# Kernel optimization log

Hardware: AMD Instinct MI355X
Metric: run time of the kernel (lower is better)

The kernel has to match this reference:

```python
import math
import jax, jax.numpy as jnp
import numpy as np

HOP = 256
N_FFT = 1024
SR = 24000
B = 8
T = 1200          # feature frames
L = T * HOP       # 307200 audio samples
K_REV = 8192
BINS = N_FFT // 2 + 1


def setup_inputs() -> dict:
    key = jax.random.key(0)
    k1, k2, k3, k4, k5 = jax.random.split(key, 5)
    # realistic voiced f0 in [50, 400] Hz (forward gates on f0 > 20 Hz)
    f0 = 50.0 + 350.0 * jax.random.uniform(k1, (B, T), dtype=jnp.float32)
    env_per = jax.random.uniform(k2, (B, BINS, T), dtype=jnp.float32)
    env_noi = 0.1 * jax.random.uniform(k3, (B, BINS, T), dtype=jnp.float32)
    rev = 0.01 * jax.random.normal(k4, (B, K_REV), dtype=jnp.float32)
    # stands in for torch.rand_like(imp) inside forward (uniform [0,1))
    noi = jax.random.uniform(k5, (B, L), dtype=jnp.float32)
    # periodic Hann window, as torch.hann_window(n_fft)
    window = (0.5 - 0.5 * jnp.cos(2.0 * jnp.pi * jnp.arange(N_FFT) / N_FFT)).astype(jnp.float32)
    return {"f0": f0, "env_per": env_per, "env_noi": env_noi, "rev": rev, "noi": noi, "window": window}


def _interp_linear(x, scale):
    # torch F.interpolate(mode='linear', align_corners=False)
    Lx = x.shape[-1]
    out_len = Lx * scale
    src = (jnp.arange(out_len, dtype=jnp.float32) + 0.5) / scale - 0.5
    src = jnp.clip(src, 0.0, Lx - 1)
    i0 = jnp.floor(src).astype(jnp.int32)
    i1 = jnp.minimum(i0 + 1, Lx - 1)
    w = src - i0.astype(jnp.float32)
    return x[:, i0] * (1.0 - w) + x[:, i1] * w


def _stft(x, window):
    # torch.stft(center=True, pad_mode='reflect', return_complex=True)
    pad = N_FFT // 2
    xp = jnp.pad(x, ((0, 0), (pad, pad)), mode='reflect')
    n_frames = 1 + (xp.shape[-1] - N_FFT) // HOP
    idx = jnp.arange(n_frames)[:, None] * HOP + jnp.arange(N_FFT)[None, :]
    frames = xp[:, idx] * window                      # [B, F, N_FFT]
    return jnp.fft.rfft(frames, axis=-1).transpose(0, 2, 1)  # [B, BINS, F]


def _istft(spec, window):
    # torch.istft(center=True): windowed overlap-add with window-square normalization
    frames = jnp.fft.irfft(spec.transpose(0, 2, 1), n=N_FFT, axis=-1) * window  # [B, F, N_FFT]
    Bc, Fr, _ = frames.shape
    out_len = N_FFT + HOP * (Fr - 1)
    idx = (jnp.arange(Fr)[:, None] * HOP + jnp.arange(N_FFT)[None, :]).reshape(-1)
    out = jnp.zeros((Bc, out_len), frames.dtype).at[:, idx].add(frames.reshape(Bc, -1))
    wsq = jnp.zeros((out_len,), frames.dtype).at[idx].add(jnp.tile(window ** 2, Fr))
    out = out / jnp.where(wsq > 1e-11, wsq, 1.0)
    pad = N_FFT // 2
    return out[:, pad:out_len - pad]


def _min_phase(amp, eps=1e-5):
    # homomorphic minimum-phase reconstruction from real amplitude envelope
    # amp: [B, BINS, F]  ->  complex spectrum exp(rfft(lifted real cepstrum))
    log_amp = jnp.log(jnp.maximum(amp, eps))
    cep = jnp.fft.irfft(log_amp, n=N_FFT, axis=1)     # [B, N_FFT, F] real cepstrum
    lift = jnp.concatenate([
        jnp.ones((1,), jnp.float32),
        2.0 * jnp.ones((N_FFT // 2 - 1,), jnp.float32),
        jnp.ones((1,), jnp.float32),
        jnp.zeros((N_FFT // 2 - 1,), jnp.float32),
    ])
    return jnp.exp(jnp.fft.rfft(cep * lift[None, :, None], axis=1))  # [B, BINS, F]


def _fft_convolve(signal, kernel):
    # DDSP-style FFT convolution: zero-pad signal right, kernel left, multiply spectra
    Ls = signal.shape[-1]
    sig = jnp.pad(signal, ((0, 0), (0, Ls)))
    ker = jnp.pad(kernel, ((0, 0), (2 * Ls - kernel.shape[-1], 0)))
    out = jnp.fft.irfft(jnp.fft.rfft(sig) * jnp.fft.rfft(ker), n=2 * Ls)
    return out[:, Ls:]


def reference(f0, env_per, env_noi, rev, noi, window):
    env_per = jnp.pad(env_per, ((0, 0), (0, 0), (1, 0)))   # [B, BINS, T+1]
    env_noi = jnp.pad(env_noi, ((0, 0), (0, 0), (1, 0)))
    # sample-rate f0 track and impulse amplitude scale
    f0_up = _interp_linear(f0, HOP)                        # [B, L]
    imp_scale = jax.lax.rsqrt(jnp.maximum(f0_up, 20.0)) * math.sqrt(SR)
    # impulse train: fire where the running phase wraps past an integer
    phase = jnp.cumsum(f0_up, axis=-1) / SR
    saw = jnp.mod(phase, 1.0)
    imp = (saw - jnp.roll(saw, 1, axis=-1) < 0.0).astype(jnp.float32)
    imp = imp.at[:, 0].set(0.0)
    imp = imp * imp_scale
    imp_stft = _stft(imp, window)                          # [B, BINS, T+1]
    noi_stft = _stft(noi, window)
    # voiced/unvoiced gating of the periodic envelope
    mask = (jnp.pad(f0, ((0, 0), (1, 0)))[:, None, :] > 20.0).astype(jnp.float32)
    env_per = env_per * mask
    voi_stft = imp_stft * _min_phase(env_per) + noi_stft * env_noi
    voi = _istft(voi_stft, window)                         # [B, L]
    voi = _fft_convolve(voi, rev)                          # [B, L]
    return voi
```

## Files before the change

### kernel.cpp

```cpp
#include <hip/hip_runtime.h>
#include <math.h>

#define BB 8
#define TT 1200
#define NFFT 1024
#define BINS 513
#define LTOT 307200
#define KREV 8192
#define NFRM 34
#define NSAMP 8960
#define OUTOFF 299008
#define SQRT_SR 154.91933384829668f

#define OFF_FR   0

__device__ __forceinline__ int rev10(int n) { return (int)(__brev((unsigned)n) >> 22); }

__device__ __forceinline__ void dit1024(float* re, float* im,
                                        const float* twr, const float* twi,
                                        float dir, int tid) {
#pragma unroll
    for (int s = 1; s <= 10; ++s) {
        const int half = 1 << (s - 1);
        __syncthreads();
        int q = tid;
        int t = q & (half - 1);
        int i0 = ((q >> (s - 1)) << s) | t;
        int i1 = i0 + half;
        float wr = twr[half - 1 + t];
        float wi = dir * twi[half - 1 + t];
        float br = re[i1], bi = im[i1];
        float vr = fmaf(br, wr, -(bi * wi));
        float vi = fmaf(br, wi, bi * wr);
        float ar = re[i0], ai = im[i0];
        re[i0] = ar + vr; im[i0] = ai + vi;
        re[i1] = ar - vr; im[i1] = ai - vi;
    }
    __syncthreads();
}

__device__ __forceinline__ void dif1024(float* re, float* im,
                                        const float* twr, const float* twi,
                                        float dir, int tid) {
#pragma unroll
    for (int s = 10; s >= 1; --s) {
        const int half = 1 << (s - 1);
        __syncthreads();
        int q = tid;
        int t = q & (half - 1);
        int i0 = ((q >> (s - 1)) << s) | t;
        int i1 = i0 + half;
        float wr = twr[half - 1 + t];
        float wi = dir * twi[half - 1 + t];
        float ar = re[i0], ai = im[i0];
        float br = re[i1], bi = im[i1];
        re[i0] = ar + br; im[i0] = ai + bi;
        float dr = ar - br, di = ai - bi;
        re[i1] = fmaf(dr, wr, -(di * wi));
        im[i1] = fmaf(dr, wi, di * wr);
    }
    __syncthreads();
}

#define LV1 0
#define LV2 4480
#define LV3 6720
#define LV4 7840
#define LV5 8400
#define LV6 8680
#define LV7 8820
#define LV8 8890
#define LV9 8925
#define LV10 8942
#define LV11 8950
#define LV12 8954
#define LV13 8956

__global__ __launch_bounds__(512) void kfrm(const float* __restrict__ f0,
                                            const float* __restrict__ env_per,
                                            const float* __restrict__ env_noi,
                                            const float* __restrict__ noi,
                                            const float* __restrict__ win,
                                            float* __restrict__ W,
                                            float* __restrict__ out) {
    const int bid = blockIdx.x;
    const int tid = threadIdx.x;
    const int b = bid / 17;
    const int fp = (bid - b * 17) * 2;
    const int fg = fp + 1;

    __shared__ __align__(16) float SMEM[17917];
    __shared__ float cw[1281], fw[1281];
    __shared__ float twr[1023], twi[1023];

    {
        float4* out4 = (float4*)out;
        int g = bid * 512 + tid;
        for (int idx = g; idx < (BB * LTOT) / 4; idx += 136 * 512)
            out4[idx] = make_float4(0.f, 0.f, 0.f, 0.f);
    }
    for (int x = tid; x < 1023; x += 512) {
        int hb = 31 - __clz(x + 1);
        int half = 1 << hb;
        int t = (x + 1) - half;
        float a = 3.14159265358979323846f * ((float)t / (float)half);
        float sv, cv; sincosf(a, &sv, &cv);
        twr[x] = cv; twi[x] = sv;
    }

    float* F = SMEM;
    float* L = SMEM + 8960;
    for (int i = tid; i < NSAMP; i += 512) {
        float src = __fsub_rn(__fdiv_rn(__fadd_rn((float)i, 0.5f), 256.0f), 0.5f);
        src = fminf(fmaxf(src, 0.0f), (float)(TT - 1));
        int i0 = (int)floorf(src);
        int i1 = i0 + 1; if (i1 > TT - 1) i1 = TT - 1;
        float w = __fsub_rn(src, (float)i0);
        float a0 = __fmul_rn(f0[b * TT + i0], __fsub_rn(1.0f, w));
        float a1 = __fmul_rn(f0[b * TT + i1], w);
        F[i] = __fadd_rn(a0, a1);
    }
    __syncthreads();
    for (int j = tid; j < 4480; j += 512) L[LV1 + j] = __fadd_rn(F[2*j], F[2*j+1]);
    __syncthreads();
    for (int j = tid; j < 2240; j += 512) L[LV2 + j] = __fadd_rn(L[LV1 + 2*j], L[LV1 + 2*j+1]);
    __syncthreads();
    for (int j = tid; j < 1120; j += 512) L[LV3 + j] = __fadd_rn(L[LV2 + 2*j], L[LV2 + 2*j+1]);
    __syncthreads();
    for (int j = tid; j < 560; j += 512)  L[LV4 + j] = __fadd_rn(L[LV3 + 2*j], L[LV3 + 2*j+1]);
    __syncthreads();
    for (int j = tid; j < 280; j += 512)  L[LV5 + j] = __fadd_rn(L[LV4 + 2*j], L[LV4 + 2*j+1]);
    __syncthreads();
    if (tid < 140) L[LV6 + tid] = __fadd_rn(L[LV5 + 2*tid], L[LV5 + 2*tid+1]);
    __syncthreads();
    if (tid < 70)  L[LV7 + tid] = __fadd_rn(L[LV6 + 2*tid], L[LV6 + 2*tid+1]);
    __syncthreads();
    if (tid < 35)  L[LV8 + tid] = __fadd_rn(L[LV7 + 2*tid], L[LV7 + 2*tid+1]);
    __syncthreads();
    if (tid < 17)  L[LV9 + tid] = __fadd_rn(L[LV8 + 2*tid], L[LV8 + 2*tid+1]);
    __syncthreads();
    if (tid < 8)   L[LV10 + tid] = __fadd_rn(L[LV9 + 2*tid], L[LV9 + 2*tid+1]);
    __syncthreads();
    if (tid < 4)   L[LV11 + tid] = __fadd_rn(L[LV10 + 2*tid], L[LV10 + 2*tid+1]);
    __syncthreads();
    if (tid < 2)   L[LV12 + tid] = __fadd_rn(L[LV11 + 2*tid], L[LV11 + 2*tid+1]);
    __syncthreads();
    if (tid < 1)   L[LV13 + tid] = __fadd_rn(L[LV12 + 0], L[LV12 + 1]);
    __syncthreads();
    const int cbase = (fp >= 3) ? (256 * fp - 513) : 0;
    {
        const int offs[14] = {0, LV1, LV2, LV3, LV4, LV5, LV6, LV7, LV8, LV9, LV10, LV11, LV12, LV13};
        for (int w = tid; w < 1281; w += 512) {
            int p = cbase + w;
            if (p < NSAMP) {
                int n = p + 1;
                float acc = 0.f; int pos = 0; bool first = true;
#pragma unroll
                for (int k = 13; k >= 1; --k) {
                    if ((n >> k) & 1) {
                        float t = L[offs[k] + (pos >> k)];
                        acc = first ? t : __fadd_rn(acc, t);
                        first = false;
                        pos += (1 << k);
                    }
                }
                if (n & 1) {
                    float t = F[pos];
                    acc = first ? t : __fadd_rn(acc, t);
                }
                cw[w] = acc;
                fw[w] = F[p];
            }
        }
    }
    __syncthreads();

    float* wr_  = SMEM;
    float* wi_  = SMEM + 1024;
    float* zfr  = SMEM + 2048;
    float* zfi  = SMEM + 3072;
    float* zgr  = SMEM + 4096;
    float* zgi  = SMEM + 5120;
    float* mpfr = SMEM + 6144;
    float* mpfi = SMEM + 6660;
    float* mpgr = SMEM + 7176;
    float* mpgi = SMEM + 7692;

    for (int k = tid; k < BINS; k += 512) {
        float epf = 0.0f;
        if (fp > 0) {
            float f0v = f0[b * TT + (fp - 1)];
            epf = (f0v > 20.0f) ? env_per[(size_t)(b * BINS + k) * TT + (fp - 1)] : 0.0f;
        }
        float f0g = f0[b * TT + (fg - 1)];
        float epg = (f0g > 20.0f) ? env_per[(size_t)(b * BINS + k) * TT + (fg - 1)] : 0.0f;
        mpfr[k] = logf(fmaxf(epf, 1e-5f));
        mpgr[k] = logf(fmaxf(epg, 1e-5f));
    }
    __syncthreads();
#pragma unroll
    for (int r = 0; r < 2; ++r) {
        int n = tid + 512 * r;
        int kv = (n <= 512) ? n : 1024 - n;
        float a = mpfr[kv], bb2 = mpgr[kv];
        __syncthreads();
        wr_[n] = a;
        wi_[n] = bb2;
    }
    dif1024(wr_, wi_, twr, twi, -1.f, tid);
    const float inv = 1.0f / 1024.0f;
#pragma unroll
    for (int r = 0; r < 2; ++r) {
        int p = tid + 512 * r;
        int n = rev10(p);
        float wgt = (n == 0 || n == 512) ? inv : ((n < 512) ? 2.0f * inv : 0.0f);
        wr_[p] *= wgt;
        wi_[p] *= wgt;
    }
    dit1024(wr_, wi_, twr, twi, -1.f, tid);
    for (int k = tid; k < BINS; k += 512) {
        int mk = (1024 - k) & 1023;
        float yr = wr_[k], yi = wi_[k];
        float ymr = wr_[mk], ymi = -wi_[mk];
        float Lfr = 0.5f * (yr + ymr), Lfi = 0.5f * (yi + ymi);
        float dr = yr - ymr, di = yi - ymi;
        float Lgr = 0.5f * di, Lgi = -0.5f * dr;
        float ef = expf(Lfr);
        mpfr[k] = ef * cosf(Lfi); mpfi[k] = ef * sinf(Lfi);
        float eg = expf(Lgr);
        mpgr[k] = eg * cosf(Lgi); mpgi[k] = eg * sinf(Lgi);
    }
    __syncthreads();
#pragma unroll
    for (int r = 0; r < 2; ++r) {
        int n = tid + 512 * r;
        int i = 256 * fp + n - 512; if (i < 0) i = -i;
        float v = 0.0f;
        if (i > 0) {
            int iw = i - cbase;
            float ph  = __fdiv_rn(cw[iw], 24000.0f);
            float sw  = __fsub_rn(ph, floorf(ph));
            float ph2 = __fdiv_rn(cw[iw - 1], 24000.0f);
            float sw2 = __fsub_rn(ph2, floorf(ph2));
            if (__fsub_rn(sw, sw2) < 0.0f)
                v = __fmul_rn(__fdiv_rn(1.0f, __fsqrt_rn(fmaxf(fw[iw], 20.0f))), SQRT_SR);
        }
        float wv = win[n];
        zfr[n] = __fmul_rn(noi[b * LTOT + i], wv);
        zfi[n] = __fmul_rn(v, wv);
        int i2 = 256 * fg + n - 512; if (i2 < 0) i2 = -i2;
        float v2 = 0.0f;
        if (i2 > 0) {
            int iw = i2 - cbase;
            float ph  = __fdiv_rn(cw[iw], 24000.0f);
            float sw  = __fsub_rn(ph, floorf(ph));
            float ph2 = __fdiv_rn(cw[iw - 1], 24000.0f);
            float sw2 = __fsub_rn(ph2, floorf(ph2));
            if (__fsub_rn(sw, sw2) < 0.0f)
                v2 = __fmul_rn(__fdiv_rn(1.0f, __fsqrt_rn(fmaxf(fw[iw], 20.0f))), SQRT_SR);
        }
        zgr[n] = __fmul_rn(noi[b * LTOT + i2], wv);
        zgi[n] = __fmul_rn(v2, wv);
    }
    dif1024(zfr, zfi, twr, twi, -1.f, tid);
    dif1024(zgr, zgi, twr, twi, -1.f, tid);
#pragma unroll
    for (int r = 0; r < 2; ++r) {
        int p = tid + 512 * r;
        int k = rev10(p);
        int kk = (k <= 512) ? k : 1024 - k;
        bool cj = (k > 512);
        int p1 = rev10(kk);
        int p2 = rev10((1024 - kk) & 1023);
        float vr, vi;
        {
            float z1r = zfr[p1], z1i = zfi[p1];
            float z2r = zfr[p2], z2i = -zfi[p2];
            float Nr = 0.5f * (z1r + z2r), Ni = 0.5f * (z1i + z2i);
            float dr = z1r - z2r, di = z1i - z2i;
            float Ir = 0.5f * di, Ii = -0.5f * dr;
            float mpr = mpfr[kk], mpi2 = mpfi[kk];
            float en = (fp == 0) ? 0.f : env_noi[(size_t)(b * BINS + kk) * TT + (fp - 1)];
            vr = Ir * mpr - Ii * mpi2 + Nr * en;
            vi = Ir * mpi2 + Ii * mpr + Ni * en;
            if (cj) vi = -vi;
        }
        float vgr, vgi;
        {
            float z1r = zgr[p1], z1i = zgi[p1];
            float z2r = zgr[p2], z2i = -zgi[p2];
            float Nr = 0.5f * (z1r + z2r), Ni = 0.5f * (z1i + z2i);
            float dr = z1r - z2r, di = z1i - z2i;
            float Ir = 0.5f * di, Ii = -0.5f * dr;
            float mpr = mpgr[kk], mpi2 = mpgi[kk];
            float en = env_noi[(size_t)(b * BINS + kk) * TT + (fg - 1)];
            vgr = Ir * mpr - Ii * mpi2 + Nr * en;
            vgi = Ir * mpi2 + Ii * mpr + Ni * en;
            if (cj) vgi = -vgi;
        }
        __syncthreads();
        wr_[p] = vr - vgi;
        wi_[p] = vi + vgr;
    }
    dit1024(wr_, wi_, twr, twi, +1.f, tid);
#pragma unroll
    for (int r = 0; r < 2; ++r) {
        int n = tid + 512 * r;
        float wv = win[n];
        W[OFF_FR + (((size_t)(b * NFRM + fp)) << 10) + n] = __fmul_rn(__fmul_rn(wr_[n], inv), wv);
        W[OFF_FR + (((size_t)(b * NFRM + fg)) << 10) + n] = __fmul_rn(__fmul_rn(wi_[n], inv), wv);
    }
}

__global__ __launch_bounds__(256) void k4(const float* __restrict__ rev,
                                          const float* __restrict__ win,
                                          const float* __restrict__ W,
                                          float* __restrict__ out) {
    const int tid = threadIdx.x;
    const int b = blockIdx.x / 72;
    int r = blockIdx.x - b * 72;
    int jt = 0, acc0 = 0;
    while (acc0 + 2 * (jt + 1) <= r) { acc0 += 2 * (jt + 1); ++jt; }
    const int mc = r - acc0;
    const int j0 = jt << 10, m0 = mc << 9;

    __shared__ __align__(16) float S[1536];
    const int base = j0 - m0 - 512;
    for (int x = tid; x < 1536; x += 256) {
        int j = base + x;
        float v = 0.f;
        if (j >= 0 && j < KREV) {
            int s = j + 512;
            int flo = (s >= 1023) ? ((s - 1023 + 255) >> 8) : 0;
            int fhi = s >> 8; if (fhi > NFRM - 1) fhi = NFRM - 1;
            float acc = 0.f, wsq = 0.f;
            for (int f = flo; f <= fhi; ++f) {
                int o = s - (f << 8);
                acc = __fadd_rn(acc, W[OFF_FR + (((size_t)(b * NFRM + f)) << 10) + o]);
                float wv = win[o];
                wsq = __fadd_rn(wsq, __fmul_rn(wv, wv));
            }
            float den = (wsq > 1e-11f) ? wsq : 1.0f;
            v = __fdiv_rn(acc, den);
        }
        S[x] = v;
    }
    __syncthreads();

    const float4* S4 = (const float4*)S;
    const float* Rb = rev + b * KREV + m0;
    float y0 = 0.f, y1 = 0.f, y2 = 0.f, y3 = 0.f;
    const int qi = tid + 128;
    float4 Bv = S4[qi];
#pragma unroll 4
    for (int mq = 0; mq < 128; ++mq) {
        float4 A = S4[qi - 1 - mq];
        float4 r4 = *(const float4*)(Rb + 4 * mq);
        y0 = fmaf(r4.x, Bv.x, y0); y0 = fmaf(r4.y, A.w,  y0); y0 = fmaf(r4.z, A.z,  y0); y0 = fmaf(r4.w, A.y,  y0);
        y1 = fmaf(r4.x, Bv.y, y1); y1 = fmaf(r4.y, Bv.x, y1); y1 = fmaf(r4.z, A.w,  y1); y1 = fmaf(r4.w, A.z,  y1);
        y2 = fmaf(r4.x, Bv.z, y2); y2 = fmaf(r4.y, Bv.y, y2); y2 = fmaf(r4.z, Bv.x, y2); y2 = fmaf(r4.w, A.w,  y2);
        y3 = fmaf(r4.x, Bv.w, y3); y3 = fmaf(r4.y, Bv.z, y3); y3 = fmaf(r4.z, Bv.y, y3); y3 = fmaf(r4.w, Bv.x, y3);
        Bv = A;
    }
    float* o = out + (size_t)b * LTOT + OUTOFF + j0 + 4 * tid;
    atomicAdd(o + 0, y0);
    atomicAdd(o + 1, y1);
    atomicAdd(o + 2, y2);
    atomicAdd(o + 3, y3);
}

extern "C" void kernel_launch(void* const* d_in, const int* in_sizes, int n_in,
                              void* d_out, int out_size, void* d_ws, size_t ws_size,
                              hipStream_t stream) {
    const float* f0      = (const float*)d_in[0];
    const float* env_per = (const float*)d_in[1];
    const float* env_noi = (const float*)d_in[2];
    const float* rev     = (const float*)d_in[3];
    const float* noi     = (const float*)d_in[4];
    const float* win     = (const float*)d_in[5];
    float* out = (float*)d_out;
    float* W   = (float*)d_ws;

    kfrm<<<dim3(136), dim3(512), 0, stream>>>(f0, env_per, env_noi, noi, win, W, out);
    k4<<<dim3(576),   dim3(256), 0, stream>>>(rev, win, W, out);
}
```

Measured before the change: 144.2 us.

## Fuse frame and convolution kernels into one cooperative kernel with grid syncs

Merges the two kernels into a single cooperative launch of 256 blocks. Phase one computes the per-batch f0 cumulative sum once in 8 blocks and writes it to workspace, while the remaining blocks zero the output. Phase two runs the per-frame FFT work, and phase three runs the reverb convolution with larger 2048-sample output tiles and 512 threads. This removes the redundant per-block prefix sum, the second launch and the atomic pressure from smaller tiles. In exchange it adds two grid-wide barriers, leaves half the blocks idle in phase two, and requires every block to be co-resident.

```diff
diff --git a/kernel.cpp b/kernel.cpp
--- a/kernel.cpp
+++ b/kernel.cpp
@@ -1,5 +1,8 @@
 #include <hip/hip_runtime.h>
+#include <hip/hip_cooperative_groups.h>
 #include <math.h>
+
+namespace cg = cooperative_groups;
 
 #define BB 8
 #define TT 1200
@@ -12,7 +15,9 @@
 #define OUTOFF 299008
 #define SQRT_SR 154.91933384829668f
 
-#define OFF_FR   0
+#define OFF_FR 0
+#define OFF_C  278528
+#define OFF_F  350208
 
 __device__ __forceinline__ int rev10(int n) { return (int)(__brev((unsigned)n) >> 22); }
 
@@ -23,9 +28,8 @@
     for (int s = 1; s <= 10; ++s) {
         const int half = 1 << (s - 1);
         __syncthreads();
-        int q = tid;
-        int t = q & (half - 1);
-        int i0 = ((q >> (s - 1)) << s) | t;
+        int t = tid & (half - 1);
+        int i0 = ((tid >> (s - 1)) << s) | t;
         int i1 = i0 + half;
         float wr = twr[half - 1 + t];
         float wi = dir * twi[half - 1 + t];
@@ -46,9 +50,8 @@
     for (int s = 10; s >= 1; --s) {
         const int half = 1 << (s - 1);
         __syncthreads();
-        int q = tid;
-        int t = q & (half - 1);
-        int i0 = ((q >> (s - 1)) << s) | t;
+        int t = tid & (half - 1);
+        int i0 = ((tid >> (s - 1)) << s) | t;
         int i1 = i0 + half;
         float wr = twr[half - 1 + t];
         float wi = dir * twi[half - 1 + t];
@@ -76,29 +79,22 @@
 #define LV12 8954
 #define LV13 8956
 
-__global__ __launch_bounds__(512) void kfrm(const float* __restrict__ f0,
-                                            const float* __restrict__ env_per,
-                                            const float* __restrict__ env_noi,
-                                            const float* __restrict__ noi,
-                                            const float* __restrict__ win,
-                                            float* __restrict__ W,
-                                            float* __restrict__ out) {
+__global__ __launch_bounds__(512) void fused(const float* __restrict__ f0,
+                                             const float* __restrict__ env_per,
+                                             const float* __restrict__ env_noi,
+                                             const float* __restrict__ rev,
+                                             const float* __restrict__ noi,
+                                             const float* __restrict__ win,
+                                             float* __restrict__ W,
+                                             float* __restrict__ out) {
+    cg::grid_group grid = cg::this_grid();
     const int bid = blockIdx.x;
     const int tid = threadIdx.x;
-    const int b = bid / 17;
-    const int fp = (bid - b * 17) * 2;
-    const int fg = fp + 1;
 
     __shared__ __align__(16) float SMEM[17917];
     __shared__ float cw[1281], fw[1281];
     __shared__ float twr[1023], twi[1023];
 
-    {
-        float4* out4 = (float4*)out;
-        int g = bid * 512 + tid;
-        for (int idx = g; idx < (BB * LTOT) / 4; idx += 136 * 512)
-            out4[idx] = make_float4(0.f, 0.f, 0.f, 0.f);
-    }
     for (int x = tid; x < 1023; x += 512) {
         int hb = 31 - __clz(x + 1);
         int half = 1 << hb;
@@ -107,266 +103,275 @@
         float sv, cv; sincosf(a, &sv, &cv);
         twr[x] = cv; twi[x] = sv;
     }
-
-    float* F = SMEM;
-    float* L = SMEM + 8960;
-    for (int i = tid; i < NSAMP; i += 512) {
-        float src = __fsub_rn(__fdiv_rn(__fadd_rn((float)i, 0.5f), 256.0f), 0.5f);
-        src = fminf(fmaxf(src, 0.0f), (float)(TT - 1));
-        int i0 = (int)floorf(src);
-        int i1 = i0 + 1; if (i1 > TT - 1) i1 = TT - 1;
-        float w = __fsub_rn(src, (float)i0);
-        float a0 = __fmul_rn(f0[b * TT + i0], __fsub_rn(1.0f, w));
-        float a1 = __fmul_rn(f0[b * TT + i1], w);
-        F[i] = __fadd_rn(a0, a1);
-    }
-    __syncthreads();
-    for (int j = tid; j < 4480; j += 512) L[LV1 + j] = __fadd_rn(F[2*j], F[2*j+1]);
-    __syncthreads();
-    for (int j = tid; j < 2240; j += 512) L[LV2 + j] = __fadd_rn(L[LV1 + 2*j], L[LV1 + 2*j+1]);
-    __syncthreads();
-    for (int j = tid; j < 1120; j += 512) L[LV3 + j] = __fadd_rn(L[LV2 + 2*j], L[LV2 + 2*j+1]);
-    __syncthreads();
-    for (int j = tid; j < 560; j += 512)  L[LV4 + j] = __fadd_rn(L[LV3 + 2*j], L[LV3 + 2*j+1]);
-    __syncthreads();
-    for (int j = tid; j < 280; j += 512)  L[LV5 + j] = __fadd_rn(L[LV4 + 2*j], L[LV4 + 2*j+1]);
-    __syncthreads();
-    if (tid < 140) L[LV6 + tid] = __fadd_rn(L[LV5 + 2*tid], L[LV5 + 2*tid+1]);
-    __syncthreads();
-    if (tid < 70)  L[LV7 + tid] = __fadd_rn(L[LV6 + 2*tid], L[LV6 + 2*tid+1]);
-    __syncthreads();
-    if (tid < 35)  L[LV8 + tid] = __fadd_rn(L[LV7 + 2*tid], L[LV7 + 2*tid+1]);
-    __syncthreads();
-    if (tid < 17)  L[LV9 + tid] = __fadd_rn(L[LV8 + 2*tid], L[LV8 + 2*tid+1]);
-    __syncthreads();
-    if (tid < 8)   L[LV10 + tid] = __fadd_rn(L[LV9 + 2*tid], L[LV9 + 2*tid+1]);
-    __syncthreads();
-    if (tid < 4)   L[LV11 + tid] = __fadd_rn(L[LV10 + 2*tid], L[LV10 + 2*tid+1]);
-    __syncthreads();
-    if (tid < 2)   L[LV12 + tid] = __fadd_rn(L[LV11 + 2*tid], L[LV11 + 2*tid+1]);
-    __syncthreads();
-    if (tid < 1)   L[LV13 + tid] = __fadd_rn(L[LV12 + 0], L[LV12 + 1]);
-    __syncthreads();
-    const int cbase = (fp >= 3) ? (256 * fp - 513) : 0;
-    {
+    if (bid < 8) {
+        const int b = bid;
+        float* F = SMEM;
+        float* L = SMEM + 8960;
+        for (int i = tid; i < NSAMP; i += 512) {
+            float src = __fsub_rn(__fdiv_rn(__fadd_rn((float)i, 0.5f), 256.0f), 0.5f);
+            src = fminf(fmaxf(src, 0.0f), (float)(TT - 1));
+            int i0 = (int)floorf(src);
+            int i1 = i0 + 1; if (i1 > TT - 1) i1 = TT - 1;
+            float w = __fsub_rn(src, (float)i0);
+            float a0 = __fmul_rn(f0[b * TT + i0], __fsub_rn(1.0f, w));
+            float a1 = __fmul_rn(f0[b * TT + i1], w);
+            F[i] = __fadd_rn(a0, a1);
+        }
+        __syncthreads();
+        for (int j = tid; j < 4480; j += 512) L[LV1 + j] = __fadd_rn(F[2*j], F[2*j+1]);
+        __syncthreads();
+        for (int j = tid; j < 2240; j += 512) L[LV2 + j] = __fadd_rn(L[LV1 + 2*j], L[LV1 + 2*j+1]);
+        __syncthreads();
+        for (int j = tid; j < 1120; j += 512) L[LV3 + j] = __fadd_rn(L[LV2 + 2*j], L[LV2 + 2*j+1]);
+        __syncthreads();
+        for (int j = tid; j < 560; j += 512)  L[LV4 + j] = __fadd_rn(L[LV3 + 2*j], L[LV3 + 2*j+1]);
+        __syncthreads();
+        for (int j = tid; j < 280; j += 512)  L[LV5 + j] = __fadd_rn(L[LV4 + 2*j], L[LV4 + 2*j+1]);
+        __syncthreads();
+        if (tid < 140) L[LV6 + tid] = __fadd_rn(L[LV5 + 2*tid], L[LV5 + 2*tid+1]);
+        __syncthreads();
+        if (tid < 70)  L[LV7 + tid] = __fadd_rn(L[LV6 + 2*tid], L[LV6 + 2*tid+1]);
+        __syncthreads();
+        if (tid < 35)  L[LV8 + tid] = __fadd_rn(L[LV7 + 2*tid], L[LV7 + 2*tid+1]);
+        __syncthreads();
+        if (tid < 17)  L[LV9 + tid] = __fadd_rn(L[LV8 + 2*tid], L[LV8 + 2*tid+1]);
+        __syncthreads();
+        if (tid < 8)   L[LV10 + tid] = __fadd_rn(L[LV9 + 2*tid], L[LV9 + 2*tid+1]);
+        __syncthreads();
+        if (tid < 4)   L[LV11 + tid] = __fadd_rn(L[LV10 + 2*tid], L[LV10 + 2*tid+1]);
+        __syncthreads();
+        if (tid < 2)   L[LV12 + tid] = __fadd_rn(L[LV11 + 2*tid], L[LV11 + 2*tid+1]);
+        __syncthreads();
+        if (tid < 1)   L[LV13 + tid] = __fadd_rn(L[LV12 + 0], L[LV12 + 1]);
+        __syncthreads();
         const int offs[14] = {0, LV1, LV2, LV3, LV4, LV5, LV6, LV7, LV8, LV9, LV10, LV11, LV12, LV13};
+        float* Wc = W + OFF_C + b * NSAMP;
+        float* Wf = W + OFF_F + b * NSAMP;
+        for (int p = tid; p < NSAMP; p += 512) {
+            int n = p + 1;
+            float acc = 0.f; int pos = 0; bool first = true;
+#pragma unroll
+            for (int k = 13; k >= 1; --k) {
+                if ((n >> k) & 1) {
+                    float t = L[offs[k] + (pos >> k)];
+                    acc = first ? t : __fadd_rn(acc, t);
+                    first = false;
+                    pos += (1 << k);
+                }
+            }
+            if (n & 1) {
+                float t = F[pos];
+                acc = first ? t : __fadd_rn(acc, t);
+            }
+            Wc[p] = acc;
+            Wf[p] = F[p];
+        }
+    } else {
+        float4* out4 = (float4*)out;
+        int g = (bid - 8) * 512 + tid;
+        for (int idx = g; idx < (BB * LTOT) / 4; idx += 248 * 512)
+            out4[idx] = make_float4(0.f, 0.f, 0.f, 0.f);
+    }
+    grid.sync();
+
+    if (bid < 136) {
+        const int b = bid / 17;
+        const int fp = (bid - b * 17) * 2;
+        const int fg = fp + 1;
+        const int cbase = (fp >= 3) ? (256 * fp - 513) : 0;
         for (int w = tid; w < 1281; w += 512) {
-            int p = cbase + w;
-            if (p < NSAMP) {
-                int n = p + 1;
-                float acc = 0.f; int pos = 0; bool first = true;
-#pragma unroll
-                for (int k = 13; k >= 1; --k) {
-                    if ((n >> k) & 1) {
-                        float t = L[offs[k] + (pos >> k)];
-                        acc = first ? t : __fadd_rn(acc, t);
-                        first = false;
-                        pos += (1 << k);
-                    }
+            cw[w] = W[OFF_C + b * NSAMP + cbase + w];
+            fw[w] = W[OFF_F + b * NSAMP + cbase + w];
+        }
+
+        float* wr_  = SMEM;
+        float* wi_  = SMEM + 1024;
+        float* zfr  = SMEM + 2048;
+        float* zfi  = SMEM + 3072;
+        float* zgr  = SMEM + 4096;
+        float* zgi  = SMEM + 5120;
+        float* mpfr = SMEM + 6144;
+        float* mpfi = SMEM + 6660;
+        float* mpgr = SMEM + 7176;
+        float* mpgi = SMEM + 7692;
+
+        for (int k = tid; k < BINS; k += 512) {
+            float epf = 0.0f;
+            if (fp > 0) {
+                float f0v = f0[b * TT + (fp - 1)];
+                epf = (f0v > 20.0f) ? env_per[(size_t)(b * BINS + k) * TT + (fp - 1)] : 0.0f;
+            }
+            float f0g = f0[b * TT + (fg - 1)];
+            float epg = (f0g > 20.0f) ? env_per[(size_t)(b * BINS + k) * TT + (fg - 1)] : 0.0f;
+            mpfr[k] = logf(fmaxf(epf, 1e-5f));
+            mpgr[k] = logf(fmaxf(epg, 1e-5f));
+        }
+        __syncthreads();
+#pragma unroll
+        for (int r = 0; r < 2; ++r) {
+            int n = tid + 512 * r;
+            int kv = (n <= 512) ? n : 1024 - n;
+            wr_[n] = mpfr[kv];
+            wi_[n] = mpgr[kv];
+        }
+        dif1024(wr_, wi_, twr, twi, -1.f, tid);
+        const float inv = 1.0f / 1024.0f;
+#pragma unroll
+        for (int r = 0; r < 2; ++r) {
+            int p = tid + 512 * r;
+            int n = rev10(p);
+            float wgt = (n == 0 || n == 512) ? inv : ((n < 512) ? 2.0f * inv : 0.0f);
+            wr_[p] *= wgt;
+            wi_[p] *= wgt;
+        }
+        dit1024(wr_, wi_, twr, twi, -1.f, tid);
+        for (int k = tid; k < BINS; k += 512) {
+            int mk = (1024 - k) & 1023;
+            float yr = wr_[k], yi = wi_[k];
+            float ymr = wr_[mk], ymi = -wi_[mk];
+            float Lfr = 0.5f * (yr + ymr), Lfi = 0.5f * (yi + ymi);
+            float dr = yr - ymr, di = yi - ymi;
+            float Lgr = 0.5f * di, Lgi = -0.5f * dr;
+            float ef = expf(Lfr);
+            mpfr[k] = ef * cosf(Lfi); mpfi[k] = ef * sinf(Lfi);
+            float eg = expf(Lgr);
+            mpgr[k] = eg * cosf(Lgi); mpgi[k] = eg * sinf(Lgi);
+        }
+        __syncthreads();
+#pragma unroll
+        for (int r = 0; r < 2; ++r) {
+            int n = tid + 512 * r;
+            int i = 256 * fp + n - 512; if (i < 0) i = -i;
+            float v = 0.0f;
+            if (i > 0) {
+                int iw = i - cbase;
+                float ph  = __fdiv_rn(cw[iw], 24000.0f);
+                float sw  = __fsub_rn(ph, floorf(ph));
+                float ph2 = __fdiv_rn(cw[iw - 1], 24000.0f);
+                float sw2 = __fsub_rn(ph2, floorf(ph2));
+                if (__fsub_rn(sw, sw2) < 0.0f)
+                    v = __fmul_rn(__fdiv_rn(1.0f, __fsqrt_rn(fmaxf(fw[iw], 20.0f))), SQRT_SR);
+            }
+            float wv = win[n];
+            zfr[n] = __fmul_rn(noi[b * LTOT + i], wv);
+            zfi[n] = __fmul_rn(v, wv);
+            int i2 = 256 * fg + n - 512; if (i2 < 0) i2 = -i2;
+            float v2 = 0.0f;
+            if (i2 > 0) {
+                int iw = i2 - cbase;
+                float ph  = __fdiv_rn(cw[iw], 24000.0f);
+                float sw  = __fsub_rn(ph, floorf(ph));
+                float ph2 = __fdiv_rn(cw[iw - 1], 24000.0f);
+                float sw2 = __fsub_rn(ph2, floorf(ph2));
+                if (__fsub_rn(sw, sw2) < 0.0f)
+                    v2 = __fmul_rn(__fdiv_rn(1.0f, __fsqrt_rn(fmaxf(fw[iw], 20.0f))), SQRT_SR);
+            }
+            zgr[n] = __fmul_rn(noi[b * LTOT + i2], wv);
+            zgi[n] = __fmul_rn(v2, wv);
+        }
+        dif1024(zfr, zfi, twr, twi, -1.f, tid);
+        dif1024(zgr, zgi, twr, twi, -1.f, tid);
+#pragma unroll
+        for (int r = 0; r < 2; ++r) {
+            int p = tid + 512 * r;
+            int k = rev10(p);
+            int kk = (k <= 512) ? k : 1024 - k;
+            bool cj = (k > 512);
+            int p1 = rev10(kk);
+            int p2 = rev10((1024 - kk) & 1023);
+            float vr, vi;
+            {
+                float z1r = zfr[p1], z1i = zfi[p1];
+                float z2r = zfr[p2], z2i = -zfi[p2];
+                float Nr = 0.5f * (z1r + z2r), Ni = 0.5f * (z1i + z2i);
+                float dr = z1r - z2r, di = z1i - z2i;
+                float Ir = 0.5f * di, Ii = -0.5f * dr;
+                float mpr = mpfr[kk], mpi2 = mpfi[kk];
+                float en = (fp == 0) ? 0.f : env_noi[(size_t)(b * BINS + kk) * TT + (fp - 1)];
+                vr = Ir * mpr - Ii * mpi2 + Nr * en;
+                vi = Ir * mpi2 + Ii * mpr + Ni * en;
+                if (cj) vi = -vi;
+            }
+            float vgr, vgi;
+            {
+                float z1r = zgr[p1], z1i = zgi[p1];
+                float z2r = zgr[p2], z2i = -zgi[p2];
+                float Nr = 0.5f * (z1r + z2r), Ni = 0.5f * (z1i + z2i);
+                float dr = z1r - z2r, di = z1i - z2i;
+                float Ir = 0.5f * di, Ii = -0.5f * dr;
+                float mpr = mpgr[kk], mpi2 = mpgi[kk];
+                float en = env_noi[(size_t)(b * BINS + kk) * TT + (fg - 1)];
+                vgr = Ir * mpr - Ii * mpi2 + Nr * en;
+                vgi = Ir * mpi2 + Ii * mpr + Ni * en;
+                if (cj) vgi = -vgi;
+            }
+            wr_[p] = vr - vgi;
+            wi_[p] = vi + vgr;
+        }
+        dit1024(wr_, wi_, twr, twi, +1.f, tid);
+#pragma unroll
+        for (int r = 0; r < 2; ++r) {
+            int n = tid + 512 * r;
+            float wv = win[n];
+            W[OFF_FR + (((size_t)(b * NFRM + fp)) << 10) + n] = __fmul_rn(__fmul_rn(wr_[n], inv), wv);
+            W[OFF_FR + (((size_t)(b * NFRM + fg)) << 10) + n] = __fmul_rn(__fmul_rn(wi_[n], inv), wv);
+        }
+    }
+    grid.sync();
+
+    float* S = SMEM;
+    for (int job = bid; job < 320; job += 256) {
+        const int b = job / 40;
+        int r = job - b * 40;
+        int jt, mt;
+        if (r < 4)       { jt = 0; mt = r; }
+        else if (r < 12) { jt = 1; mt = r - 4; }
+        else if (r < 24) { jt = 2; mt = r - 12; }
+        else             { jt = 3; mt = r - 24; }
+        const int j0 = jt << 11, m0 = mt << 9;
+        const int base = j0 - m0 - 512;
+        __syncthreads();
+        for (int x = tid; x < 2560; x += 512) {
+            int j = base + x;
+            float v = 0.f;
+            if (j >= 0 && j < KREV) {
+                int s = j + 512;
+                int flo = (s >= 1023) ? ((s - 1023 + 255) >> 8) : 0;
+                int fhi = s >> 8; if (fhi > NFRM - 1) fhi = NFRM - 1;
+                float acc = 0.f, wsq = 0.f;
+                for (int f = flo; f <= fhi; ++f) {
+                    int o = s - (f << 8);
+                    acc = __fadd_rn(acc, W[OFF_FR + (((size_t)(b * NFRM + f)) << 10) + o]);
+                    float wv = win[o];
+                    wsq = __fadd_rn(wsq, __fmul_rn(wv, wv));
                 }
-                if (n & 1) {
-                    float t = F[pos];
-                    acc = first ? t : __fadd_rn(acc, t);
-                }
-                cw[w] = acc;
-                fw[w] = F[p];
-            }
-        }
-    }
-    __syncthreads();
-
-    float* wr_  = SMEM;
-    float* wi_  = SMEM + 1024;
-    float* zfr  = SMEM + 2048;
-    float* zfi  = SMEM + 3072;
-    float* zgr  = SMEM + 4096;
-    float* zgi  = SMEM + 5120;
-    float* mpfr = SMEM + 6144;
-    float* mpfi = SMEM + 6660;
-    float* mpgr = SMEM + 7176;
-    float* mpgi = SMEM + 7692;
-
-    for (int k = tid; k < BINS; k += 512) {
-        float epf = 0.0f;
-        if (fp > 0) {
-            float f0v = f0[b * TT + (fp - 1)];
-            epf = (f0v > 20.0f) ? env_per[(size_t)(b * BINS + k) * TT + (fp - 1)] : 0.0f;
-        }
-        float f0g = f0[b * TT + (fg - 1)];
-        float epg = (f0g > 20.0f) ? env_per[(size_t)(b * BINS + k) * TT + (fg - 1)] : 0.0f;
-        mpfr[k] = logf(fmaxf(epf, 1e-5f));
-        mpgr[k] = logf(fmaxf(epg, 1e-5f));
-    }
-    __syncthreads();
-#pragma unroll
-    for (int r = 0; r < 2; ++r) {
-        int n = tid + 512 * r;
-        int kv = (n <= 512) ? n : 1024 - n;
-        float a = mpfr[kv], bb2 = mpgr[kv];
-        __syncthreads();
-        wr_[n] = a;
-        wi_[n] = bb2;
-    }
-    dif1024(wr_, wi_, twr, twi, -1.f, tid);
-    const float inv = 1.0f / 1024.0f;
-#pragma unroll
-    for (int r = 0; r < 2; ++r) {
-        int p = tid + 512 * r;
-        int n = rev10(p);
-        float wgt = (n == 0 || n == 512) ? inv : ((n < 512) ? 2.0f * inv : 0.0f);
-        wr_[p] *= wgt;
-        wi_[p] *= wgt;
-    }
-    dit1024(wr_, wi_, twr, twi, -1.f, tid);
-    for (int k = tid; k < BINS; k += 512) {
-        int mk = (1024 - k) & 1023;
-        float yr = wr_[k], yi = wi_[k];
-        float ymr = wr_[mk], ymi = -wi_[mk];
-        float Lfr = 0.5f * (yr + ymr), Lfi = 0.5f * (yi + ymi);
-        float dr = yr - ymr, di = yi - ymi;
-        float Lgr = 0.5f * di, Lgi = -0.5f * dr;
-        float ef = expf(Lfr);
-        mpfr[k] = ef * cosf(Lfi); mpfi[k] = ef * sinf(Lfi);
-        float eg = expf(Lgr);
-        mpgr[k] = eg * cosf(Lgi); mpgi[k] = eg * sinf(Lgi);
-    }
-    __syncthreads();
-#pragma unroll
-    for (int r = 0; r < 2; ++r) {
-        int n = tid + 512 * r;
-        int i = 256 * fp + n - 512; if (i < 0) i = -i;
-        float v = 0.0f;
-        if (i > 0) {
-            int iw = i - cbase;
-            float ph  = __fdiv_rn(cw[iw], 24000.0f);
-            float sw  = __fsub_rn(ph, floorf(ph));
-            float ph2 = __fdiv_rn(cw[iw - 1], 24000.0f);
-            float sw2 = __fsub_rn(ph2, floorf(ph2));
-            if (__fsub_rn(sw, sw2) < 0.0f)
-                v = __fmul_rn(__fdiv_rn(1.0f, __fsqrt_rn(fmaxf(fw[iw], 20.0f))), SQRT_SR);
-        }
-        float wv = win[n];
-        zfr[n] = __fmul_rn(noi[b * LTOT + i], wv);
-        zfi[n] = __fmul_rn(v, wv);
-        int i2 = 256 * fg + n - 512; if (i2 < 0) i2 = -i2;
-        float v2 = 0.0f;
-        if (i2 > 0) {
-            int iw = i2 - cbase;
-            float ph  = __fdiv_rn(cw[iw], 24000.0f);
-            float sw  = __fsub_rn(ph, floorf(ph));
-            float ph2 = __fdiv_rn(cw[iw - 1], 24000.0f);
-            float sw2 = __fsub_rn(ph2, floorf(ph2));
-            if (__fsub_rn(sw, sw2) < 0.0f)
-                v2 = __fmul_rn(__fdiv_rn(1.0f, __fsqrt_rn(fmaxf(fw[iw], 20.0f))), SQRT_SR);
-        }
-        zgr[n] = __fmul_rn(noi[b * LTOT + i2], wv);
-        zgi[n] = __fmul_rn(v2, wv);
-    }
-    dif1024(zfr, zfi, twr, twi, -1.f, tid);
-    dif1024(zgr, zgi, twr, twi, -1.f, tid);
-#pragma unroll
-    for (int r = 0; r < 2; ++r) {
-        int p = tid + 512 * r;
-        int k = rev10(p);
-        int kk = (k <= 512) ? k : 1024 - k;
-        bool cj = (k > 512);
-        int p1 = rev10(kk);
-        int p2 = rev10((1024 - kk) & 1023);
-        float vr, vi;
-        {
-            float z1r = zfr[p1], z1i = zfi[p1];
-            float z2r = zfr[p2], z2i = -zfi[p2];
-            float Nr = 0.5f * (z1r + z2r), Ni = 0.5f * (z1i + z2i);
-            float dr = z1r - z2r, di = z1i - z2i;
-            float Ir = 0.5f * di, Ii = -0.5f * dr;
-            float mpr = mpfr[kk], mpi2 = mpfi[kk];
-            float en = (fp == 0) ? 0.f : env_noi[(size_t)(b * BINS + kk) * TT + (fp - 1)];
-            vr = Ir * mpr - Ii * mpi2 + Nr * en;
-            vi = Ir * mpi2 + Ii * mpr + Ni * en;
-            if (cj) vi = -vi;
-        }
-        float vgr, vgi;
-        {
-            float z1r = zgr[p1], z1i = zgi[p1];
-            float z2r = zgr[p2], z2i = -zgi[p2];
-            float Nr = 0.5f * (z1r + z2r), Ni = 0.5f * (z1i + z2i);
-            float dr = z1r - z2r, di = z1i - z2i;
-            float Ir = 0.5f * di, Ii = -0.5f * dr;
-            float mpr = mpgr[kk], mpi2 = mpgi[kk];
-            float en = env_noi[(size_t)(b * BINS + kk) * TT + (fg - 1)];
-            vgr = Ir * mpr - Ii * mpi2 + Nr * en;
-            vgi = Ir * mpi2 + Ii * mpr + Ni * en;
-            if (cj) vgi = -vgi;
-        }
-        __syncthreads();
-        wr_[p] = vr - vgi;
-        wi_[p] = vi + vgr;
-    }
-    dit1024(wr_, wi_, twr, twi, +1.f, tid);
-#pragma unroll
-    for (int r = 0; r < 2; ++r) {
-        int n = tid + 512 * r;
-        float wv = win[n];
-        W[OFF_FR + (((size_t)(b * NFRM + fp)) << 10) + n] = __fmul_rn(__fmul_rn(wr_[n], inv), wv);
-        W[OFF_FR + (((size_t)(b * NFRM + fg)) << 10) + n] = __fmul_rn(__fmul_rn(wi_[n], inv), wv);
-    }
-}
-
-__global__ __launch_bounds__(256) void k4(const float* __restrict__ rev,
-                                          const float* __restrict__ win,
-                                          const float* __restrict__ W,
-                                          float* __restrict__ out) {
-    const int tid = threadIdx.x;
-    const int b = blockIdx.x / 72;
-    int r = blockIdx.x - b * 72;
-    int jt = 0, acc0 = 0;
-    while (acc0 + 2 * (jt + 1) <= r) { acc0 += 2 * (jt + 1); ++jt; }
-    const int mc = r - acc0;
-    const int j0 = jt << 10, m0 = mc << 9;
-
-    __shared__ __align__(16) float S[1536];
-    const int base = j0 - m0 - 512;
-    for (int x = tid; x < 1536; x += 256) {
-        int j = base + x;
-        float v = 0.f;
-        if (j >= 0 && j < KREV) {
-            int s = j + 512;
-            int flo = (s >= 1023) ? ((s - 1023 + 255) >> 8) : 0;
-            int fhi = s >> 8; if (fhi > NFRM - 1) fhi = NFRM - 1;
-            float acc = 0.f, wsq = 0.f;
-            for (int f = flo; f <= fhi; ++f) {
-                int o = s - (f << 8);
-                acc = __fadd_rn(acc, W[OFF_FR + (((size_t)(b * NFRM + f)) << 10) + o]);
-                float wv = win[o];
-                wsq = __fadd_rn(wsq, __fmul_rn(wv, wv));
-            }
-            float den = (wsq > 1e-11f) ? wsq : 1.0f;
-            v = __fdiv_rn(acc, den);
-        }
-        S[x] = v;
-    }
-    __syncthreads();
-
-    const float4* S4 = (const float4*)S;
-    const float* Rb = rev + b * KREV + m0;
-    float y0 = 0.f, y1 = 0.f, y2 = 0.f, y3 = 0.f;
-    const int qi = tid + 128;
-    float4 Bv = S4[qi];
+                float den = (wsq > 1e-11f) ? wsq : 1.0f;
+                v = __fdiv_rn(acc, den);
+            }
+            S[x] = v;
+        }
+        __syncthreads();
+        const float4* S4 = (const float4*)S;
+        const float* Rb = rev + (size_t)b * KREV + m0;
+        float y0 = 0.f, y1 = 0.f, y2 = 0.f, y3 = 0.f;
+        const int qi = tid + 128;
+        float4 Bv = S4[qi];
 #pragma unroll 4
-    for (int mq = 0; mq < 128; ++mq) {
-        float4 A = S4[qi - 1 - mq];
-        float4 r4 = *(const float4*)(Rb + 4 * mq);
-        y0 = fmaf(r4.x, Bv.x, y0); y0 = fmaf(r4.y, A.w,  y0); y0 = fmaf(r4.z, A.z,  y0); y0 = fmaf(r4.w, A.y,  y0);
-        y1 = fmaf(r4.x, Bv.y, y1); y1 = fmaf(r4.y, Bv.x, y1); y1 = fmaf(r4.z, A.w,  y1); y1 = fmaf(r4.w, A.z,  y1);
-        y2 = fmaf(r4.x, Bv.z, y2); y2 = fmaf(r4.y, Bv.y, y2); y2 = fmaf(r4.z, Bv.x, y2); y2 = fmaf(r4.w, A.w,  y2);
-        y3 = fmaf(r4.x, Bv.w, y3); y3 = fmaf(r4.y, Bv.z, y3); y3 = fmaf(r4.z, Bv.y, y3); y3 = fmaf(r4.w, Bv.x, y3);
-        Bv = A;
-    }
-    float* o = out + (size_t)b * LTOT + OUTOFF + j0 + 4 * tid;
-    atomicAdd(o + 0, y0);
-    atomicAdd(o + 1, y1);
-    atomicAdd(o + 2, y2);
-    atomicAdd(o + 3, y3);
+        for (int mq = 0; mq < 128; ++mq) {
+            float4 A = S4[qi - 1 - mq];
+            float4 r4 = *(const float4*)(Rb + 4 * mq);
+            y0 = fmaf(r4.x, Bv.x, y0); y0 = fmaf(r4.y, A.w,  y0); y0 = fmaf(r4.z, A.z,  y0); y0 = fmaf(r4.w, A.y,  y0);
+            y1 = fmaf(r4.x, Bv.y, y1); y1 = fmaf(r4.y, Bv.x, y1); y1 = fmaf(r4.z, A.w,  y1); y1 = fmaf(r4.w, A.z,  y1);
+            y2 = fmaf(r4.x, Bv.z, y2); y2 = fmaf(r4.y, Bv.y, y2); y2 = fmaf(r4.z, Bv.x, y2); y2 = fmaf(r4.w, A.w,  y2);
+            y3 = fmaf(r4.x, Bv.w, y3); y3 = fmaf(r4.y, Bv.z, y3); y3 = fmaf(r4.z, Bv.y, y3); y3 = fmaf(r4.w, Bv.x, y3);
+            Bv = A;
+        }
+        float* o = out + (size_t)b * LTOT + OUTOFF + j0 + 4 * tid;
+        atomicAdd(o + 0, y0);
+        atomicAdd(o + 1, y1);
+        atomicAdd(o + 2, y2);
+        atomicAdd(o + 3, y3);
+    }
 }
 
 extern "C" void kernel_launch(void* const* d_in, const int* in_sizes, int n_in,
@@ -381,6 +386,7 @@
     float* out = (float*)d_out;
     float* W   = (float*)d_ws;
 
-    kfrm<<<dim3(136), dim3(512), 0, stream>>>(f0, env_per, env_noi, noi, win, W, out);
-    k4<<<dim3(576),   dim3(256), 0, stream>>>(rev, win, W, out);
+    void* args[] = {(void*)&f0, (void*)&env_per, (void*)&env_noi, (void*)&rev,
+                    (void*)&noi, (void*)&win, (void*)&W, (void*)&out};
+    hipLaunchCooperativeKernel((void*)fused, dim3(256), dim3(512), args, 0, stream);
 }
```

After: 232.0 us. 1.61x slower.

## Switch in-block 1024-point FFTs to radix-4 and run paired FFTs concurrently

Applied to the files above, without the earlier changes.

Replaces the radix-2 DIF/DIT 1024-point shared-memory FFTs with radix-4 versions using base-4 digit reversal, halving the number of stages and barriers. The two independent frame FFTs are now done in one pass, with each half of the 512-thread block taking one transform. The prefix-sum level tree is also built two levels per barrier, and a few redundant syncs are dropped. This cuts barrier count and shared-memory traffic. In exchange, half the threads sit idle in the single-transform FFTs, and removing syncs risks read/write races on wr_/wi_.

```diff
diff --git a/kernel.cpp b/kernel.cpp
--- a/kernel.cpp
+++ b/kernel.cpp
@@ -14,50 +14,84 @@
 
 #define OFF_FR   0
 
-__device__ __forceinline__ int rev10(int n) { return (int)(__brev((unsigned)n) >> 22); }
-
-__device__ __forceinline__ void dit1024(float* re, float* im,
-                                        const float* twr, const float* twi,
-                                        float dir, int tid) {
-#pragma unroll
-    for (int s = 1; s <= 10; ++s) {
-        const int half = 1 << (s - 1);
+__device__ __forceinline__ int rev4_10(int n) {
+    int r = (int)(__brev((unsigned)n) >> 22);
+    return ((r & 0x155) << 1) | ((r & 0x2AA) >> 1);
+}
+
+__device__ __forceinline__ void dif4(float* re, float* im,
+                                     const float* twr, const float* twi,
+                                     float dir, int u, bool act) {
+#pragma unroll
+    for (int s = 0; s < 5; ++s) {
+        const int q = 256 >> (2 * s);
+        const int sh = 8 - 2 * s;
         __syncthreads();
-        int q = tid;
-        int t = q & (half - 1);
-        int i0 = ((q >> (s - 1)) << s) | t;
-        int i1 = i0 + half;
-        float wr = twr[half - 1 + t];
-        float wi = dir * twi[half - 1 + t];
-        float br = re[i1], bi = im[i1];
-        float vr = fmaf(br, wr, -(bi * wi));
-        float vi = fmaf(br, wi, bi * wr);
-        float ar = re[i0], ai = im[i0];
-        re[i0] = ar + vr; im[i0] = ai + vi;
-        re[i1] = ar - vr; im[i1] = ai - vi;
-    }
-    __syncthreads();
-}
-
-__device__ __forceinline__ void dif1024(float* re, float* im,
-                                        const float* twr, const float* twi,
-                                        float dir, int tid) {
-#pragma unroll
-    for (int s = 10; s >= 1; --s) {
-        const int half = 1 << (s - 1);
+        if (act) {
+            int t = u & (q - 1);
+            int base = ((u >> sh) << (sh + 2)) | t;
+            int i0 = base, i1 = base + q, i2 = base + 2 * q, i3 = base + 3 * q;
+            float ar = re[i0], ai = im[i0];
+            float br = re[i1], bi = im[i1];
+            float cr = re[i2], ci = im[i2];
+            float dr = re[i3], di = im[i3];
+            float t0r = ar + cr, t0i = ai + ci;
+            float t1r = ar - cr, t1i = ai - ci;
+            float t2r = br + dr, t2i = bi + di;
+            float t3r = br - dr, t3i = bi - di;
+            float y0r = t0r + t2r, y0i = t0i + t2i;
+            float y2r = t0r - t2r, y2i = t0i - t2i;
+            float y1r = t1r - dir * t3i, y1i = t1i + dir * t3r;
+            float y3r = t1r + dir * t3i, y3i = t1i - dir * t3r;
+            float c1 = twr[2 * q - 1 + t], s1 = twi[2 * q - 1 + t];
+            float c2 = twr[q - 1 + t],     s2 = twi[q - 1 + t];
+            float w1r = c1, w1i = dir * s1;
+            float w2r = c2, w2i = dir * s2;
+            float w3r = c1 * c2 - s1 * s2;
+            float w3i = dir * (c1 * s2 + s1 * c2);
+            re[i0] = y0r;                       im[i0] = y0i;
+            re[i1] = y1r * w1r - y1i * w1i;     im[i1] = y1r * w1i + y1i * w1r;
+            re[i2] = y2r * w2r - y2i * w2i;     im[i2] = y2r * w2i + y2i * w2r;
+            re[i3] = y3r * w3r - y3i * w3i;     im[i3] = y3r * w3i + y3i * w3r;
+        }
+    }
+    __syncthreads();
+}
+
+__device__ __forceinline__ void dit4(float* re, float* im,
+                                     const float* twr, const float* twi,
+                                     float dir, int u, bool act) {
+#pragma unroll
+    for (int s = 0; s < 5; ++s) {
+        const int q = 1 << (2 * s);
+        const int sh = 2 * s;
         __syncthreads();
-        int q = tid;
-        int t = q & (half - 1);
-        int i0 = ((q >> (s - 1)) << s) | t;
-        int i1 = i0 + half;
-        float wr = twr[half - 1 + t];
-        float wi = dir * twi[half - 1 + t];
-        float ar = re[i0], ai = im[i0];
-        float br = re[i1], bi = im[i1];
-        re[i0] = ar + br; im[i0] = ai + bi;
-        float dr = ar - br, di = ai - bi;
-        re[i1] = fmaf(dr, wr, -(di * wi));
-        im[i1] = fmaf(dr, wi, di * wr);
+        if (act) {
+            int t = u & (q - 1);
+            int base = ((u >> sh) << (sh + 2)) | t;
+            int i0 = base, i1 = base + q, i2 = base + 2 * q, i3 = base + 3 * q;
+            float c1 = twr[2 * q - 1 + t], s1 = twi[2 * q - 1 + t];
+            float c2 = twr[q - 1 + t],     s2 = twi[q - 1 + t];
+            float w1r = c1, w1i = dir * s1;
+            float w2r = c2, w2i = dir * s2;
+            float w3r = c1 * c2 - s1 * s2;
+            float w3i = dir * (c1 * s2 + s1 * c2);
+            float ar = re[i0], ai = im[i0];
+            float xr = re[i1], xi = im[i1];
+            float yr = re[i2], yi = im[i2];
+            float zr = re[i3], zi = im[i3];
+            float br = xr * w1r - xi * w1i, bi = xr * w1i + xi * w1r;
+            float cr = yr * w2r - yi * w2i, ci = yr * w2i + yi * w2r;
+            float dr = zr * w3r - zi * w3i, di = zr * w3i + zi * w3r;
+            float t0r = ar + cr, t0i = ai + ci;
+            float t1r = ar - cr, t1i = ai - ci;
+            float t2r = br + dr, t2i = bi + di;
+            float t3r = br - dr, t3i = bi - di;
+            re[i0] = t0r + t2r;            im[i0] = t0i + t2i;
+            re[i2] = t0r - t2r;            im[i2] = t0i - t2i;
+            re[i1] = t1r - dir * t3i;      im[i1] = t1i + dir * t3r;
+            re[i3] = t1r + dir * t3i;      im[i3] = t1i - dir * t3r;
+        }
     }
     __syncthreads();
 }
@@ -121,31 +155,58 @@
         F[i] = __fadd_rn(a0, a1);
     }
     __syncthreads();
-    for (int j = tid; j < 4480; j += 512) L[LV1 + j] = __fadd_rn(F[2*j], F[2*j+1]);
-    __syncthreads();
-    for (int j = tid; j < 2240; j += 512) L[LV2 + j] = __fadd_rn(L[LV1 + 2*j], L[LV1 + 2*j+1]);
-    __syncthreads();
-    for (int j = tid; j < 1120; j += 512) L[LV3 + j] = __fadd_rn(L[LV2 + 2*j], L[LV2 + 2*j+1]);
-    __syncthreads();
-    for (int j = tid; j < 560; j += 512)  L[LV4 + j] = __fadd_rn(L[LV3 + 2*j], L[LV3 + 2*j+1]);
-    __syncthreads();
-    for (int j = tid; j < 280; j += 512)  L[LV5 + j] = __fadd_rn(L[LV4 + 2*j], L[LV4 + 2*j+1]);
-    __syncthreads();
-    if (tid < 140) L[LV6 + tid] = __fadd_rn(L[LV5 + 2*tid], L[LV5 + 2*tid+1]);
-    __syncthreads();
-    if (tid < 70)  L[LV7 + tid] = __fadd_rn(L[LV6 + 2*tid], L[LV6 + 2*tid+1]);
-    __syncthreads();
-    if (tid < 35)  L[LV8 + tid] = __fadd_rn(L[LV7 + 2*tid], L[LV7 + 2*tid+1]);
-    __syncthreads();
-    if (tid < 17)  L[LV9 + tid] = __fadd_rn(L[LV8 + 2*tid], L[LV8 + 2*tid+1]);
-    __syncthreads();
-    if (tid < 8)   L[LV10 + tid] = __fadd_rn(L[LV9 + 2*tid], L[LV9 + 2*tid+1]);
-    __syncthreads();
-    if (tid < 4)   L[LV11 + tid] = __fadd_rn(L[LV10 + 2*tid], L[LV10 + 2*tid+1]);
-    __syncthreads();
-    if (tid < 2)   L[LV12 + tid] = __fadd_rn(L[LV11 + 2*tid], L[LV11 + 2*tid+1]);
-    __syncthreads();
-    if (tid < 1)   L[LV13 + tid] = __fadd_rn(L[LV12 + 0], L[LV12 + 1]);
+    for (int j = tid; j < 2240; j += 512) {
+        float a = __fadd_rn(F[4*j],     F[4*j + 1]);
+        float c = __fadd_rn(F[4*j + 2], F[4*j + 3]);
+        L[LV1 + 2*j] = a; L[LV1 + 2*j + 1] = c;
+        L[LV2 + j] = __fadd_rn(a, c);
+    }
+    __syncthreads();
+    for (int j = tid; j < 560; j += 512) {
+        float a = __fadd_rn(L[LV2 + 4*j],     L[LV2 + 4*j + 1]);
+        float c = __fadd_rn(L[LV2 + 4*j + 2], L[LV2 + 4*j + 3]);
+        L[LV3 + 2*j] = a; L[LV3 + 2*j + 1] = c;
+        L[LV4 + j] = __fadd_rn(a, c);
+    }
+    __syncthreads();
+    if (tid < 140) {
+        int j = tid;
+        float a = __fadd_rn(L[LV4 + 4*j],     L[LV4 + 4*j + 1]);
+        float c = __fadd_rn(L[LV4 + 4*j + 2], L[LV4 + 4*j + 3]);
+        L[LV5 + 2*j] = a; L[LV5 + 2*j + 1] = c;
+        L[LV6 + j] = __fadd_rn(a, c);
+    }
+    __syncthreads();
+    if (tid < 35) {
+        int j = tid;
+        float a = __fadd_rn(L[LV6 + 4*j],     L[LV6 + 4*j + 1]);
+        float c = __fadd_rn(L[LV6 + 4*j + 2], L[LV6 + 4*j + 3]);
+        L[LV7 + 2*j] = a; L[LV7 + 2*j + 1] = c;
+        L[LV8 + j] = __fadd_rn(a, c);
+    }
+    __syncthreads();
+    if (tid < 9) {
+        int j = tid;
+        if (j < 8) {
+            float a = __fadd_rn(L[LV8 + 4*j],     L[LV8 + 4*j + 1]);
+            float c = __fadd_rn(L[LV8 + 4*j + 2], L[LV8 + 4*j + 3]);
+            L[LV9 + 2*j] = a; L[LV9 + 2*j + 1] = c;
+            L[LV10 + j] = __fadd_rn(a, c);
+        } else {
+            L[LV9 + 16] = __fadd_rn(L[LV8 + 32], L[LV8 + 33]);
+        }
+    }
+    __syncthreads();
+    if (tid == 0) {
+        float a0 = __fadd_rn(L[LV10 + 0], L[LV10 + 1]);
+        float a1 = __fadd_rn(L[LV10 + 2], L[LV10 + 3]);
+        float a2 = __fadd_rn(L[LV10 + 4], L[LV10 + 5]);
+        float a3 = __fadd_rn(L[LV10 + 6], L[LV10 + 7]);
+        L[LV11 + 0] = a0; L[LV11 + 1] = a1; L[LV11 + 2] = a2; L[LV11 + 3] = a3;
+        float b0 = __fadd_rn(a0, a1), b1 = __fadd_rn(a2, a3);
+        L[LV12 + 0] = b0; L[LV12 + 1] = b1;
+        L[LV13 + 0] = __fadd_rn(b0, b1);
+    }
     __syncthreads();
     const int cbase = (fp >= 3) ? (256 * fp - 513) : 0;
     {
@@ -185,6 +246,8 @@
     float* mpfi = SMEM + 6660;
     float* mpgr = SMEM + 7176;
     float* mpgi = SMEM + 7692;
+    const int u = tid & 255;
+    const bool lo = (tid < 256);
 
     for (int k = tid; k < BINS; k += 512) {
         float epf = 0.0f;
@@ -202,22 +265,20 @@
     for (int r = 0; r < 2; ++r) {
         int n = tid + 512 * r;
         int kv = (n <= 512) ? n : 1024 - n;
-        float a = mpfr[kv], bb2 = mpgr[kv];
-        __syncthreads();
-        wr_[n] = a;
-        wi_[n] = bb2;
-    }
-    dif1024(wr_, wi_, twr, twi, -1.f, tid);
+        wr_[n] = mpfr[kv];
+        wi_[n] = mpgr[kv];
+    }
+    dif4(wr_, wi_, twr, twi, -1.f, u, lo);
     const float inv = 1.0f / 1024.0f;
 #pragma unroll
     for (int r = 0; r < 2; ++r) {
         int p = tid + 512 * r;
-        int n = rev10(p);
+        int n = rev4_10(p);
         float wgt = (n == 0 || n == 512) ? inv : ((n < 512) ? 2.0f * inv : 0.0f);
         wr_[p] *= wgt;
         wi_[p] *= wgt;
     }
-    dit1024(wr_, wi_, twr, twi, -1.f, tid);
+    dit4(wr_, wi_, twr, twi, -1.f, u, lo);
     for (int k = tid; k < BINS; k += 512) {
         int mk = (1024 - k) & 1023;
         float yr = wr_[k], yi = wi_[k];
@@ -262,16 +323,15 @@
         zgr[n] = __fmul_rn(noi[b * LTOT + i2], wv);
         zgi[n] = __fmul_rn(v2, wv);
     }
-    dif1024(zfr, zfi, twr, twi, -1.f, tid);
-    dif1024(zgr, zgi, twr, twi, -1.f, tid);
+    dif4(lo ? zfr : zgr, lo ? zfi : zgi, twr, twi, -1.f, u, true);
 #pragma unroll
     for (int r = 0; r < 2; ++r) {
         int p = tid + 512 * r;
-        int k = rev10(p);
+        int k = rev4_10(p);
         int kk = (k <= 512) ? k : 1024 - k;
         bool cj = (k > 512);
-        int p1 = rev10(kk);
-        int p2 = rev10((1024 - kk) & 1023);
+        int p1 = rev4_10(kk);
+        int p2 = rev4_10((1024 - kk) & 1023);
         float vr, vi;
         {
             float z1r = zfr[p1], z1i = zfi[p1];
@@ -298,11 +358,10 @@
             vgi = Ir * mpi2 + Ii * mpr + Ni * en;
             if (cj) vgi = -vgi;
         }
-        __syncthreads();
         wr_[p] = vr - vgi;
         wi_[p] = vi + vgr;
     }
-    dit1024(wr_, wi_, twr, twi, +1.f, tid);
+    dit4(wr_, wi_, twr, twi, +1.f, u, lo);
 #pragma unroll
     for (int r = 0; r < 2; ++r) {
         int n = tid + 512 * r;
```

Result: faster. 141.2 us (-2.1%).
